# Optimization experiments

Measured on AMD Instinct MI355X. Metric: run time of the kernel, lower is better.

The kernel has to match this reference:

```python
import jax, jax.numpy as jnp
import numpy as np

N_NODES = 100000
N_EDGES = 1600000
D = 128


def setup_inputs() -> dict:
    key = jax.random.key(0)
    ks = jax.random.split(key, 6)
    x = jax.random.normal(ks[0], (N_NODES, D), dtype=jnp.float32)
    src = jax.random.randint(ks[1], (N_EDGES,), 0, N_NODES, dtype=jnp.int32)
    dst = jax.random.randint(ks[2], (N_EDGES,), 0, N_NODES, dtype=jnp.int32)
    # Xavier-ish small weights
    W1 = jax.random.normal(ks[3], (D, D), dtype=jnp.float32) * 0.05
    W2 = jax.random.normal(ks[4], (D, D), dtype=jnp.float32) * 0.05
    b1 = jnp.zeros((D,), dtype=jnp.float32)
    b2 = jnp.zeros((D,), dtype=jnp.float32)
    prelu_a = jnp.full((1,), 0.25, dtype=jnp.float32)  # nn.PReLU default, shared across layers
    return {"x": x, "src": src, "dst": dst, "W1": W1, "b1": b1, "W2": W2, "b2": b2, "prelu_a": prelu_a}


def reference(x, src, dst, W1, b1, W2, b2, prelu_a):
    N = x.shape[0]
    # DGL GraphConv norm='left': scale source features by 1/clamp(out_degree, 1)
    deg = jax.ops.segment_sum(jnp.ones(src.shape, x.dtype), src, num_segments=N)
    inv_outdeg = (1.0 / jnp.maximum(deg, 1.0))[:, None]  # [N,1]

    def layer(h, W, b):
        h = h * inv_outdeg                                   # left-normalize sources
        agg = jax.ops.segment_sum(h[src], dst, num_segments=N)  # SpMM: sum messages at dst
        z = agg @ W + b                                      # dense transform (aggregate-first since in==out feats)
        return jnp.where(z >= 0, z, prelu_a * z)             # shared PReLU

    z = layer(x, W1, b1)
    z = layer(z, W2, b2)
    return z
```

## Files before the change

kernel.cpp:

```cpp
#include <hip/hip_runtime.h>

#define D 128
#define CAP 64
#define PADR 136

#define BSHIFT 7
#define NCH 256
#define BSTRIDE_LOG 12

typedef short short8 __attribute__((ext_vector_type(8)));
typedef float floatx4 __attribute__((ext_vector_type(4)));

static __device__ __forceinline__ unsigned short f2bf(float f) {
    unsigned int u = __float_as_uint(f);
    u += 0x7fffu + ((u >> 16) & 1u);
    return (unsigned short)(u >> 16);
}
static __device__ __forceinline__ unsigned int pack2bf(float a, float b) {
    return (unsigned int)f2bf(a) | ((unsigned int)f2bf(b) << 16);
}
static __device__ __forceinline__ int rd16(const unsigned int* __restrict__ pc, int v) {
    return (int)((pc[v >> 1] >> ((v & 1) * 16)) & 0xffffu);
}
static __device__ __forceinline__ void acc8(float* a, uint4 v) {
    a[0] += __uint_as_float(v.x << 16);  a[1] += __uint_as_float(v.x & 0xffff0000u);
    a[2] += __uint_as_float(v.y << 16);  a[3] += __uint_as_float(v.y & 0xffff0000u);
    a[4] += __uint_as_float(v.z << 16);  a[5] += __uint_as_float(v.z & 0xffff0000u);
    a[6] += __uint_as_float(v.w << 16);  a[7] += __uint_as_float(v.w & 0xffff0000u);
}

__global__ __launch_bounds__(512) void k_cnt(const int* __restrict__ dst,
                                             unsigned int* __restrict__ gcnt,
                                             unsigned int* __restrict__ pcnt_out,
                                             int E, int cs, int nbuck, int npc) {
    __shared__ unsigned int h[1024];
    int b = blockIdx.x, t = threadIdx.x;
    for (int i = b * 512 + t; i < npc; i += NCH * 512) pcnt_out[i] = 0;
    for (int k = t; k < nbuck; k += 512) h[k] = 0;
    __syncthreads();
    int lo = b * cs, hi = lo + cs;
    if (hi > E) hi = E;
#pragma unroll 4
    for (int e = lo + t; e < hi; e += 512)
        atomicAdd(&h[(unsigned)dst[e] >> BSHIFT], 1u);
    __syncthreads();
    for (int k = t; k < nbuck; k += 512) gcnt[(size_t)b * nbuck + k] = h[k];
}

__global__ __launch_bounds__(NCH) void k_pfx1(unsigned int* __restrict__ gcnt,
                                              unsigned int* __restrict__ btot, int nbuck) {
    __shared__ unsigned int sa[NCH], sb[NCH];
    int k = blockIdx.x, t = threadIdx.x;
    unsigned int v = gcnt[(size_t)t * nbuck + k];
    sa[t] = v;
    unsigned int* A = sa; unsigned int* B = sb;
    for (int off = 1; off < NCH; off <<= 1) {
        __syncthreads();
        B[t] = A[t] + ((t >= off) ? A[t - off] : 0u);
        unsigned int* tmp = A; A = B; B = tmp;
    }
    __syncthreads();
    unsigned int incl = A[t];
    gcnt[(size_t)t * nbuck + k] = incl - v;
    if (t == NCH - 1) btot[k] = incl;
}

__global__ __launch_bounds__(512) void k_scat(const int* __restrict__ src, const int* __restrict__ dst,
                                              const unsigned int* __restrict__ goff,
                                              unsigned int* __restrict__ pcnt_out,
                                              unsigned int* __restrict__ bdata,
                                              int E, int cs, int nbuck) {
    __shared__ unsigned int cur[1024];
    int b = blockIdx.x, t = threadIdx.x;
    for (int k = t; k < nbuck; k += 512)
        cur[k] = ((unsigned int)k << BSTRIDE_LOG) + goff[(size_t)b * nbuck + k];
    __syncthreads();
    int lo = b * cs, hi = lo + cs;
    if (hi > E) hi = E;
#pragma unroll 2
    for (int e = lo + t; e < hi; e += 512) {
        int s = src[e];
        int d = dst[e];
        atomicAdd(&pcnt_out[s >> 1], 1u << ((s & 1) * 16));
        unsigned int kb = (unsigned)d >> BSHIFT;
        unsigned int p = atomicAdd(&cur[kb], 1u);
        if (p < ((kb + 1u) << BSTRIDE_LOG))
            bdata[p] = ((unsigned int)(d & ((1 << BSHIFT) - 1)) << 17) | (unsigned int)s;
    }
}

__global__ __launch_bounds__(256) void k_csrprep(
    const unsigned int* __restrict__ bdata, const unsigned int* __restrict__ btot,
    unsigned int* __restrict__ pcnt_in, int* __restrict__ esrc,
    const float* __restrict__ x, const unsigned int* __restrict__ pcnt_out,
    float* __restrict__ inv, uint2* __restrict__ xb2, int total4,
    const float* __restrict__ W1, const float* __restrict__ W2,
    unsigned short* __restrict__ WT1, unsigned short* __restrict__ WT2,
    uint4* __restrict__ z0, uint4* __restrict__ z1,
    int n, int nbuck) {
    __shared__ unsigned int lcnt[128];
    int b = blockIdx.x;

    if (b < nbuck) {
        int base = b << BSHIFT;
        if (threadIdx.x < 128) lcnt[threadIdx.x] = 0;
        __syncthreads();
        int lo = b << BSTRIDE_LOG;
        int cnt = (int)btot[b];
        if (cnt > (1 << BSTRIDE_LOG)) cnt = 1 << BSTRIDE_LOG;
        for (int i = threadIdx.x; i < cnt; i += 256) {
            unsigned int e = bdata[lo + i];
            int s = (int)(e & 0x1FFFFu);
            int dl = (int)(e >> 17);
            unsigned int p = atomicAdd(&lcnt[dl], 1u);
            if (p < CAP) esrc[((size_t)(base + dl) << 6) + p] = s;
        }
        __syncthreads();
        if (threadIdx.x < 128) {
            int node = base + threadIdx.x;
            if (node < n) {
                int c = (int)lcnt[threadIdx.x];
                if (c > CAP) c = CAP;
                int cp = (c + 7) & ~7;
                for (int p = c; p < cp; p++)
                    esrc[((size_t)node << 6) + p] = n;
            }
        }
        if (threadIdx.x < 64) {
            int node0 = base + threadIdx.x * 2;
            if (node0 < n) {
                unsigned int c0 = lcnt[threadIdx.x * 2];
                unsigned int c1 = lcnt[threadIdx.x * 2 + 1];
                pcnt_in[(base >> 1) + threadIdx.x] = (c0 & 0xffffu) | (c1 << 16);
            }
        }
        return;
    }

    int bb = b - nbuck;
    int nb4 = (total4 + 255) >> 8;
    if (bb >= nb4 + 128) {
        if (threadIdx.x < 16) z0[threadIdx.x] = (uint4){0u, 0u, 0u, 0u};
        else if (threadIdx.x < 32) z1[threadIdx.x - 16] = (uint4){0u, 0u, 0u, 0u};
        return;
    }
    if (bb >= nb4) {
        int wb = bb - nb4;
        const float* W = (wb < 64) ? W1 : W2;
        unsigned short* WT = (wb < 64) ? WT1 : WT2;
        int idx = (wb & 63) * 256 + threadIdx.x;
        int k = idx >> 7, nn = idx & 127;
        WT[nn * 128 + k] = f2bf(W[idx]);
        return;
    }
    int i = bb * 256 + threadIdx.x;
    if (i >= total4) return;
    int row = i >> 5;
    int d = rd16(pcnt_out, row);
    float s = 1.0f / (float)(d > 1 ? d : 1);
    if ((i & 31) == 0) inv[row] = s;
    float4 v = ((const float4*)x)[i];
    uint2 o;
    o.x = pack2bf(v.x * s, v.y * s);
    o.y = pack2bf(v.z * s, v.w * s);
    xb2[i] = o;
}

template<bool OUTBF>
__global__ __launch_bounds__(256) void k_fused(
    const uint4* __restrict__ hb4, const unsigned int* __restrict__ pcnt_in,
    const int* __restrict__ esrc, const unsigned short* __restrict__ WT,
    const float* __restrict__ bias, const float* __restrict__ pa,
    const float* __restrict__ inv, void* __restrict__ outp, int n)
{
    __shared__ unsigned short sAgg[16 * PADR];
    int wv = threadIdx.x >> 6;
    int lane = threadIdx.x & 63;
    int q = lane >> 4;
    int f = lane & 15;
    int nb = blockIdx.x * 16;

    for (int ii = 0; ii < 4; ii += 2) {
        int nodeA = nb + wv * 4 + ii;
        int nodeB = nodeA + 1;
        int cA = (nodeA < n) ? rd16(pcnt_in, nodeA) : 0;
        int cB = (nodeB < n) ? rd16(pcnt_in, nodeB) : 0;
        if (cA > CAP) cA = CAP;
        if (cB > CAP) cB = CAP;
        cA = (cA + 7) & ~7;
        cB = (cB + 7) & ~7;
        const int* epA = esrc + ((size_t)nodeA << 6);
        const int* epB = esrc + ((size_t)nodeB << 6);
        float accA[8], accB[8];
#pragma unroll
        for (int j = 0; j < 8; j++) { accA[j] = 0.f; accB[j] = 0.f; }
        int mx = cA > cB ? cA : cB;
        for (int base = 0; base < mx; base += 8) {
            bool dA = base < cA, dB = base < cB;
            int2 eA, eB;
            uint4 vA0, vA1, vB0, vB1;
            if (dA) eA = *(const int2*)(epA + base + 2 * q);
            if (dB) eB = *(const int2*)(epB + base + 2 * q);
            if (dA) { vA0 = hb4[(size_t)eA.x * 16 + f]; vA1 = hb4[(size_t)eA.y * 16 + f]; }
            if (dB) { vB0 = hb4[(size_t)eB.x * 16 + f]; vB1 = hb4[(size_t)eB.y * 16 + f]; }
            if (dA) { acc8(accA, vA0); acc8(accA, vA1); }
            if (dB) { acc8(accB, vB0); acc8(accB, vB1); }
        }
#pragma unroll
        for (int j = 0; j < 8; j++) {
            accA[j] += __shfl_xor(accA[j], 16, 64);
            accA[j] += __shfl_xor(accA[j], 32, 64);
            accB[j] += __shfl_xor(accB[j], 16, 64);
            accB[j] += __shfl_xor(accB[j], 32, 64);
        }
        if (q == 0) {
            uint4 oA, oB;
            oA.x = pack2bf(accA[0], accA[1]); oA.y = pack2bf(accA[2], accA[3]);
            oA.z = pack2bf(accA[4], accA[5]); oA.w = pack2bf(accA[6], accA[7]);
            oB.x = pack2bf(accB[0], accB[1]); oB.y = pack2bf(accB[2], accB[3]);
            oB.z = pack2bf(accB[4], accB[5]); oB.w = pack2bf(accB[6], accB[7]);
            if (nodeA < n) *(uint4*)&sAgg[(wv * 4 + ii) * PADR + f * 8] = oA;
            if (nodeB < n) *(uint4*)&sAgg[(wv * 4 + ii + 1) * PADR + f * 8] = oB;
        }
    }
    __syncthreads();

    int m = lane & 15;
    short8 a0 = *(const short8*)&sAgg[m * PADR +   0 + q * 8];
    short8 a1 = *(const short8*)&sAgg[m * PADR +  32 + q * 8];
    short8 a2 = *(const short8*)&sAgg[m * PADR +  64 + q * 8];
    short8 a3 = *(const short8*)&sAgg[m * PADR +  96 + q * 8];

    float alpha = pa[0];
    float* outf = (float*)outp;
    unsigned short* outb = (unsigned short*)outp;

    float invr[4];
    if (OUTBF) {
#pragma unroll
        for (int r = 0; r < 4; r++) {
            int row = nb + q * 4 + r;
            invr[r] = (row < n) ? inv[row] : 1.f;
        }
    }

#pragma unroll
    for (int tt = 0; tt < 2; tt++) {
        int t = wv * 2 + tt;
        int col = t * 16 + m;
        const short8* Bp = (const short8*)(WT + (size_t)col * 128 + q * 8);
        floatx4 acc = {0.f, 0.f, 0.f, 0.f};
        acc = __builtin_amdgcn_mfma_f32_16x16x32_bf16(a0, Bp[0],  acc, 0, 0, 0);
        acc = __builtin_amdgcn_mfma_f32_16x16x32_bf16(a1, Bp[4],  acc, 0, 0, 0);
        acc = __builtin_amdgcn_mfma_f32_16x16x32_bf16(a2, Bp[8],  acc, 0, 0, 0);
        acc = __builtin_amdgcn_mfma_f32_16x16x32_bf16(a3, Bp[12], acc, 0, 0, 0);
        float bb = bias[col];
#pragma unroll
        for (int r = 0; r < 4; r++) {
            int row = nb + q * 4 + r;
            if (row < n) {
                float z = acc[r] + bb;
                z = (z >= 0.f) ? z : alpha * z;
                if (OUTBF)
                    outb[(size_t)row * 128 + col] = f2bf(z * invr[r]);
                else
                    __builtin_nontemporal_store(z, &outf[(size_t)row * 128 + col]);
            }
        }
    }
}

__global__ __launch_bounds__(256) void k_gather(
    const uint4* __restrict__ hb4, const unsigned int* __restrict__ pcnt_in,
    const int* __restrict__ esrc, uint4* __restrict__ aggb4, int n)
{
    int lane = threadIdx.x & 63;
    int node = blockIdx.x * 4 + (threadIdx.x >> 6);
    if (node >= n) return;
    int q = lane >> 4, f = lane & 15;
    int cnt = rd16(pcnt_in, node);
    if (cnt > CAP) cnt = CAP;
    cnt = (cnt + 7) & ~7;
    const int* ep = esrc + ((size_t)node << 6);

    float acc[8];
#pragma unroll
    for (int j = 0; j < 8; j++) acc[j] = 0.f;

    for (int base = 0; base < cnt; base += 8) {
        int2 e = *(const int2*)(ep + base + 2 * q);
        uint4 v0 = hb4[(size_t)e.x * 16 + f];
        uint4 v1 = hb4[(size_t)e.y * 16 + f];
        acc8(acc, v0);
        acc8(acc, v1);
    }
#pragma unroll
    for (int j = 0; j < 8; j++) {
        acc[j] += __shfl_xor(acc[j], 16, 64);
        acc[j] += __shfl_xor(acc[j], 32, 64);
    }
    if (q == 0) {
        uint4 o;
        o.x = pack2bf(acc[0], acc[1]);
        o.y = pack2bf(acc[2], acc[3]);
        o.z = pack2bf(acc[4], acc[5]);
        o.w = pack2bf(acc[6], acc[7]);
        aggb4[(size_t)node * 16 + f] = o;
    }
}

__global__ __launch_bounds__(256) void k_gemm(
    const unsigned short* __restrict__ A, const unsigned short* __restrict__ WT,
    const float* __restrict__ bias, const float* __restrict__ pa,
    float* __restrict__ outf, int n)
{
    int lane = threadIdx.x & 63;
    int wv = threadIdx.x >> 6;
    int m = lane & 15, q = lane >> 4;
    int mbase = blockIdx.x * 64 + wv * 16;
    int arow = mbase + m;
    if (arow > n - 1) arow = n - 1;

    const short8* Ap = (const short8*)(A + (size_t)arow * 128 + q * 8);
    short8 a0 = Ap[0], a1 = Ap[4], a2 = Ap[8], a3 = Ap[12];

    float alpha = pa[0];
#pragma unroll
    for (int t = 0; t < 8; t++) {
        int col = t * 16 + m;
        const short8* Bp = (const short8*)(WT + (size_t)col * 128 + q * 8);
        floatx4 acc = {0.f, 0.f, 0.f, 0.f};
        acc = __builtin_amdgcn_mfma_f32_16x16x32_bf16(a0, Bp[0],  acc, 0, 0, 0);
        acc = __builtin_amdgcn_mfma_f32_16x16x32_bf16(a1, Bp[4],  acc, 0, 0, 0);
        acc = __builtin_amdgcn_mfma_f32_16x16x32_bf16(a2, Bp[8],  acc, 0, 0, 0);
        acc = __builtin_amdgcn_mfma_f32_16x16x32_bf16(a3, Bp[12], acc, 0, 0, 0);
        float bb = bias[col];
#pragma unroll
        for (int r = 0; r < 4; r++) {
            int row = mbase + q * 4 + r;
            if (row < n) {
                float z = acc[r] + bb;
                z = (z >= 0.f) ? z : alpha * z;
                outf[(size_t)row * 128 + col] = z;
            }
        }
    }
}

extern "C" void kernel_launch(void* const* d_in, const int* in_sizes, int n_in,
                              void* d_out, int out_size, void* d_ws, size_t ws_size,
                              hipStream_t stream) {
    const float* x   = (const float*)d_in[0];
    const int* src   = (const int*)d_in[1];
    const int* dst   = (const int*)d_in[2];
    const float* W1  = (const float*)d_in[3];
    const float* b1  = (const float*)d_in[4];
    const float* W2  = (const float*)d_in[5];
    const float* b2  = (const float*)d_in[6];
    const float* pa  = (const float*)d_in[7];
    float* out = (float*)d_out;

    const int N = in_sizes[0] / D;
    const int E = in_sizes[1];

    char* ws = (char*)d_ws;
    size_t off = 0;
    unsigned short* buf0 = (unsigned short*)(ws + off); off += (size_t)(N + 1) * D * 2;
    unsigned short* buf1 = (unsigned short*)(ws + off); off += (size_t)(N + 1) * D * 2;
    const size_t pc_words = (size_t)((N + 1) / 2);
    unsigned int* pcnt_out = (unsigned int*)(ws + off); off += pc_words * 4;
    unsigned int* pcnt_in  = (unsigned int*)(ws + off); off += pc_words * 4;
    float* inv   = (float*)(ws + off); off += (size_t)N * sizeof(float);
    unsigned short* WT1 = (unsigned short*)(ws + off); off += 128 * 128 * 2;
    unsigned short* WT2 = (unsigned short*)(ws + off); off += 128 * 128 * 2;
    size_t off_esrc = off;
    size_t need_big = off_esrc + (size_t)N * CAP * sizeof(int);
    bool big = (ws_size >= need_big);

    int* esrc = big ? (int*)(ws + off_esrc) : (int*)d_out;

    const int nbuck = (N + (1 << BSHIFT) - 1) >> BSHIFT;
    unsigned int* bdata  = (unsigned int*)buf1;
    unsigned int* gcnt   = bdata + ((size_t)nbuck << BSTRIDE_LOG);
    unsigned int* btot   = gcnt + (size_t)NCH * nbuck;

    const int cs = (E + NCH - 1) / NCH;
    const int total4 = N * (D / 4);
    uint4* z0 = (uint4*)(buf0 + (size_t)N * D);
    uint4* z1 = (uint4*)(buf1 + (size_t)N * D);

    k_cnt <<<NCH, 512, 0, stream>>>(dst, gcnt, pcnt_out, E, cs, nbuck, (int)pc_words);
    k_pfx1<<<nbuck, NCH, 0, stream>>>(gcnt, btot, nbuck);
    k_scat<<<NCH, 512, 0, stream>>>(src, dst, gcnt, pcnt_out, bdata, E, cs, nbuck);

    const int nb4 = (total4 + 255) / 256;
    const int NBC = nbuck + nb4 + 128 + 1;
    k_csrprep<<<NBC, 256, 0, stream>>>(bdata, btot, pcnt_in, esrc,
                                       x, pcnt_out, inv, (uint2*)buf0, total4,
                                       W1, W2, WT1, WT2, z0, z1, N, nbuck);

    const int NBF = (N + 15) / 16;

    k_fused<true><<<NBF, 256, 0, stream>>>((const uint4*)buf0, pcnt_in, esrc, WT1, b1, pa, inv,
                                           (void*)buf1, N);

    if (big) {
        k_fused<false><<<NBF, 256, 0, stream>>>((const uint4*)buf1, pcnt_in, esrc, WT2, b2, pa, inv,
                                                (void*)out, N);
    } else {
        const int NBG = (N + 3) / 4;
        const int NBM = (N + 63) / 64;
        k_gather<<<NBG, 256, 0, stream>>>((const uint4*)buf1, pcnt_in, esrc, (uint4*)buf0, N);
        k_gemm<<<NBM, 256, 0, stream>>>(buf0, WT2, b2, pa, out, N);
    }
}
```

Baseline: 380.4 us.

## Use coarser dst buckets, more chunks, and move out-degree count into count pass

Raises the destination bucket size from 128 to 512 nodes and the chunk count from 256 to 512, which shrinks the number of buckets and the per-chunk histogram and prefix work. The out-degree atomics move from the scatter pass into the count pass, and zeroing of the degree array becomes a separate memset. The CSR-prep kernel loops over the larger bucket with 256 threads. Larger buckets mean fewer blocks in CSR prep and more shared-atomic contention per bucket, and the memset adds one more launch.

```diff
diff --git a/kernel.cpp b/kernel.cpp
--- a/kernel.cpp
+++ b/kernel.cpp
@@ -4,9 +4,9 @@
 #define CAP 64
 #define PADR 136
 
-#define BSHIFT 7
-#define NCH 256
-#define BSTRIDE_LOG 12
+#define BSHIFT 9
+#define NCH 512
+#define BSTRIDE_LOG 14
 
 typedef short short8 __attribute__((ext_vector_type(8)));
 typedef float floatx4 __attribute__((ext_vector_type(4)));
@@ -29,20 +29,22 @@
     a[6] += __uint_as_float(v.w << 16);  a[7] += __uint_as_float(v.w & 0xffff0000u);
 }
 
-__global__ __launch_bounds__(512) void k_cnt(const int* __restrict__ dst,
+__global__ __launch_bounds__(512) void k_cnt(const int* __restrict__ src,
+                                             const int* __restrict__ dst,
                                              unsigned int* __restrict__ gcnt,
                                              unsigned int* __restrict__ pcnt_out,
-                                             int E, int cs, int nbuck, int npc) {
-    __shared__ unsigned int h[1024];
+                                             int E, int cs, int nbuck) {
+    __shared__ unsigned int h[512];
     int b = blockIdx.x, t = threadIdx.x;
-    for (int i = b * 512 + t; i < npc; i += NCH * 512) pcnt_out[i] = 0;
     for (int k = t; k < nbuck; k += 512) h[k] = 0;
     __syncthreads();
     int lo = b * cs, hi = lo + cs;
     if (hi > E) hi = E;
-#pragma unroll 4
-    for (int e = lo + t; e < hi; e += 512)
+    for (int e = lo + t; e < hi; e += 512) {
         atomicAdd(&h[(unsigned)dst[e] >> BSHIFT], 1u);
+        int s = src[e];
+        atomicAdd(&pcnt_out[s >> 1], 1u << ((s & 1) * 16));
+    }
     __syncthreads();
     for (int k = t; k < nbuck; k += 512) gcnt[(size_t)b * nbuck + k] = h[k];
 }
@@ -67,21 +69,18 @@
 
 __global__ __launch_bounds__(512) void k_scat(const int* __restrict__ src, const int* __restrict__ dst,
                                               const unsigned int* __restrict__ goff,
-                                              unsigned int* __restrict__ pcnt_out,
                                               unsigned int* __restrict__ bdata,
                                               int E, int cs, int nbuck) {
-    __shared__ unsigned int cur[1024];
+    __shared__ unsigned int cur[512];
     int b = blockIdx.x, t = threadIdx.x;
     for (int k = t; k < nbuck; k += 512)
         cur[k] = ((unsigned int)k << BSTRIDE_LOG) + goff[(size_t)b * nbuck + k];
     __syncthreads();
     int lo = b * cs, hi = lo + cs;
     if (hi > E) hi = E;
-#pragma unroll 2
     for (int e = lo + t; e < hi; e += 512) {
         int s = src[e];
         int d = dst[e];
-        atomicAdd(&pcnt_out[s >> 1], 1u << ((s & 1) * 16));
         unsigned int kb = (unsigned)d >> BSHIFT;
         unsigned int p = atomicAdd(&cur[kb], 1u);
         if (p < ((kb + 1u) << BSTRIDE_LOG))
@@ -98,12 +97,12 @@
     unsigned short* __restrict__ WT1, unsigned short* __restrict__ WT2,
     uint4* __restrict__ z0, uint4* __restrict__ z1,
     int n, int nbuck) {
-    __shared__ unsigned int lcnt[128];
+    __shared__ unsigned int lcnt[1 << BSHIFT];
     int b = blockIdx.x;
 
     if (b < nbuck) {
         int base = b << BSHIFT;
-        if (threadIdx.x < 128) lcnt[threadIdx.x] = 0;
+        for (int k = threadIdx.x; k < (1 << BSHIFT); k += 256) lcnt[k] = 0;
         __syncthreads();
         int lo = b << BSTRIDE_LOG;
         int cnt = (int)btot[b];
@@ -116,22 +115,22 @@
             if (p < CAP) esrc[((size_t)(base + dl) << 6) + p] = s;
         }
         __syncthreads();
-        if (threadIdx.x < 128) {
-            int node = base + threadIdx.x;
+        for (int nn = threadIdx.x; nn < (1 << BSHIFT); nn += 256) {
+            int node = base + nn;
             if (node < n) {
-                int c = (int)lcnt[threadIdx.x];
+                int c = (int)lcnt[nn];
                 if (c > CAP) c = CAP;
                 int cp = (c + 7) & ~7;
                 for (int p = c; p < cp; p++)
                     esrc[((size_t)node << 6) + p] = n;
             }
         }
-        if (threadIdx.x < 64) {
-            int node0 = base + threadIdx.x * 2;
+        for (int tt = threadIdx.x; tt < (1 << (BSHIFT - 1)); tt += 256) {
+            int node0 = base + tt * 2;
             if (node0 < n) {
-                unsigned int c0 = lcnt[threadIdx.x * 2];
-                unsigned int c1 = lcnt[threadIdx.x * 2 + 1];
-                pcnt_in[(base >> 1) + threadIdx.x] = (c0 & 0xffffu) | (c1 << 16);
+                unsigned int c0 = lcnt[tt * 2];
+                unsigned int c1 = lcnt[tt * 2 + 1];
+                pcnt_in[(base >> 1) + tt] = (c0 & 0xffffu) | (c1 << 16);
             }
         }
         return;
@@ -389,9 +388,11 @@
     uint4* z0 = (uint4*)(buf0 + (size_t)N * D);
     uint4* z1 = (uint4*)(buf1 + (size_t)N * D);
 
-    k_cnt <<<NCH, 512, 0, stream>>>(dst, gcnt, pcnt_out, E, cs, nbuck, (int)pc_words);
+    hipMemsetAsync(pcnt_out, 0, pc_words * 4, stream);
+
+    k_cnt <<<NCH, 512, 0, stream>>>(src, dst, gcnt, pcnt_out, E, cs, nbuck);
     k_pfx1<<<nbuck, NCH, 0, stream>>>(gcnt, btot, nbuck);
-    k_scat<<<NCH, 512, 0, stream>>>(src, dst, gcnt, pcnt_out, bdata, E, cs, nbuck);
+    k_scat<<<NCH, 512, 0, stream>>>(src, dst, gcnt, bdata, E, cs, nbuck);
 
     const int nb4 = (total4 + 255) / 256;
     const int NBC = nbuck + nb4 + 128 + 1;
```

Measured after the change: 380.7 us. No clear change (+0.1%).
